# Kernel optimization log

Hardware: AMD Instinct MI355X
Metric: run time of the kernel (lower is better)

The kernel has to match this reference:

```python
import jax, jax.numpy as jnp
import numpy as np

B, IN, H = 16384, 1024, 1024


def setup_inputs() -> dict:
    key = jax.random.key(0)
    ks = jax.random.split(key, 16)
    stdv = 1.0 / np.sqrt(H)
    u = lambda k, shape: jax.random.uniform(k, shape, jnp.float32, -stdv, stdv)
    return {
        "input": jax.random.normal(ks[0], (B, IN), jnp.float32),
        "prev_h": jax.random.normal(ks[1], (B, H), jnp.float32),
        "prev_c": jax.random.normal(ks[2], (B, H), jnp.float32),
        "weight_xi": u(ks[3], (IN, H)), "weight_hi": u(ks[4], (H, H)),
        "weight_xf": u(ks[5], (IN, H)), "weight_hf": u(ks[6], (H, H)),
        "weight_xu": u(ks[7], (IN, H)), "weight_hu": u(ks[8], (H, H)),
        "weight_xo": u(ks[9], (IN, H)), "weight_ho": u(ks[10], (H, H)),
        "bias_i": u(ks[11], (H,)), "bias_f": u(ks[12], (H,)),
        "bias_o": u(ks[13], (H,)), "bias_u": u(ks[14], (H,)),
    }


def reference(input, prev_h, prev_c,
              weight_xi, weight_hi, weight_xf, weight_hf,
              weight_xu, weight_hu, weight_xo, weight_ho,
              bias_i, bias_f, bias_o, bias_u):
    i = jax.nn.sigmoid(input @ weight_xi + prev_h @ weight_hi + bias_i)
    f = jax.nn.sigmoid(input @ weight_xf + prev_h @ weight_hf + bias_f)
    o = jax.nn.sigmoid(input @ weight_xo + prev_h @ weight_ho + bias_o)
    u = jnp.tanh(input @ weight_xu + prev_h @ weight_hu + bias_u)
    c = f * prev_c + i * u
    h = o * jnp.tanh(c)
    return (h, c)
```

## Files before the change

kernel.cpp:

```cpp
#include <hip/hip_runtime.h>
#include <hip/hip_bf16.h>
#include <stdint.h>
#include <type_traits>


typedef short bf16x8 __attribute__((ext_vector_type(8)));
typedef unsigned short u16x8 __attribute__((ext_vector_type(8)));
typedef float f32x4 __attribute__((ext_vector_type(4)));

__device__ __forceinline__ unsigned short f2bf(float f) {
    union { float f; uint32_t u; } v; v.f = f;
    uint32_t r = v.u + 0x7FFFu + ((v.u >> 16) & 1u);
    return (unsigned short)(r >> 16);
}

__device__ __forceinline__ float fsig(float x) { return 1.0f / (1.0f + __expf(-x)); }
__device__ __forceinline__ float ftanh(float x) { return 2.0f * fsig(2.0f * x) - 1.0f; }

__global__ __launch_bounds__(256) void pack_a_kernel(const float* __restrict__ input,
                                                     const float* __restrict__ prev_h,
                                                     unsigned short* __restrict__ Apk) {
    long idx = (long)blockIdx.x * 256 + threadIdx.x;
    long e0 = idx * 8;
    int b = (int)(e0 >> 11);
    int k = (int)(e0 & 2047);
    const float* src = (k < 1024) ? (input + (size_t)b * 1024 + k)
                                  : (prev_h + (size_t)b * 1024 + (k - 1024));
    float4 lo = *(const float4*)src;
    float4 hi = *(const float4*)(src + 4);
    u16x8 o;
    o[0] = f2bf(lo.x); o[1] = f2bf(lo.y); o[2] = f2bf(lo.z); o[3] = f2bf(lo.w);
    o[4] = f2bf(hi.x); o[5] = f2bf(hi.y); o[6] = f2bf(hi.z); o[7] = f2bf(hi.w);
    *(u16x8*)(Apk + e0) = o;
}

__global__ __launch_bounds__(256) void pack_b_kernel(
        const float* __restrict__ wxi, const float* __restrict__ wxf,
        const float* __restrict__ wxo, const float* __restrict__ wxu,
        const float* __restrict__ whi, const float* __restrict__ whf,
        const float* __restrict__ who, const float* __restrict__ whu,
        unsigned short* __restrict__ Bpk) {
    int idx = blockIdx.x * 256 + threadIdx.x;
    int g  = idx >> 18;
    int r  = idx & 262143;
    int kc = r >> 10;
    int j  = r & 1023;
    const float* wx = (g == 0) ? wxi : (g == 1) ? wxf : (g == 2) ? wxo : wxu;
    const float* wh = (g == 0) ? whi : (g == 1) ? whf : (g == 2) ? who : whu;
    int k0 = kc * 8;
    const float* src = (k0 < 1024) ? (wx + (size_t)k0 * 1024 + j)
                                   : (wh + (size_t)(k0 - 1024) * 1024 + j);
    u16x8 o;
#pragma unroll
    for (int t = 0; t < 8; ++t) o[t] = f2bf(src[(size_t)t * 1024]);
    *(u16x8*)(Bpk + (((size_t)(g * 1024 + j)) << 11) + k0) = o;
}


#define GLL(gp, lp) __builtin_amdgcn_global_load_lds( \
        (__attribute__((address_space(1))) void*)(gp), \
        (__attribute__((address_space(3))) void*)(lp), 16, 0, 0)

#define BAR() do { asm volatile("" ::: "memory"); __builtin_amdgcn_s_barrier(); \
                   asm volatile("" ::: "memory"); } while (0)

__global__ __launch_bounds__(512, 2) void lstm_gemm_kernel(
        const unsigned short* __restrict__ Apk,
        const unsigned short* __restrict__ Bpk,
        const float* __restrict__ prev_c,
        const float* __restrict__ bi, const float* __restrict__ bf_,
        const float* __restrict__ bo, const float* __restrict__ bu,
        float* __restrict__ out_h, float* __restrict__ out_c) {
    __shared__ __align__(16) unsigned char smem[131072];
    const int tid = threadIdx.x;
    const int w = tid >> 6, l = tid & 63;
    const int lr = l & 15, s4 = l >> 4;
    const int wm = w >> 2, wq = w & 3;

    const int bid = blockIdx.x;
    const int sw = ((bid & 7) << 7) + (bid >> 3);
    const int tileRow = sw & 63, tileCol = sw >> 6;
    const int rowBase = tileRow * 256;
    const int jBase = tileCol * 64;

    const int swr = ((s4 ^ ((lr >> 1) & 3)) << 4);

    int aoff[8], boff[4];
#pragma unroll
    for (int m = 0; m < 8; ++m) aoff[m] = (wm * 128 + m * 16 + lr) * 64 + swr;
#pragma unroll
    for (int g = 0; g < 4; ++g) boff[g] = 16384 + (g * 64 + wq * 16 + lr) * 64 + swr;

    const int slot = (l & 3) ^ ((l >> 3) & 3);
    const int rloc = w * 16 + (l >> 2);
    const unsigned short* aSrc0 = Apk + (size_t)(rowBase + rloc) * 2048 + slot * 8;
    const unsigned short* aSrc1 = Apk + (size_t)(rowBase + 128 + rloc) * 2048 + slot * 8;
    const int br0 = rloc, br1 = 128 + rloc;
    const unsigned short* bSrc0 = Bpk + (((size_t)((br0 >> 6) * 1024 + jBase + (br0 & 63))) << 11) + slot * 8;
    const unsigned short* bSrc1 = Bpk + (((size_t)((br1 >> 6) * 1024 + jBase + (br1 & 63))) << 11) + slot * 8;
    const int aDst0 = w * 1024;
    const int aDst1 = 8192 + w * 1024;
    const int bDst0 = 16384 + w * 1024;
    const int bDst1 = 24576 + w * 1024;

#define STAGE_A2(T) do { const int _bb = ((T) & 3) * 32768; \
        GLL(aSrc0 + (size_t)(T) * 32, smem + _bb + aDst0); \
        GLL(aSrc1 + (size_t)(T) * 32, smem + _bb + aDst1); } while (0)
#define STAGE_B2(T) do { const int _bb = ((T) & 3) * 32768; \
        GLL(bSrc0 + (size_t)(T) * 32, smem + _bb + bDst0); \
        GLL(bSrc1 + (size_t)(T) * 32, smem + _bb + bDst1); } while (0)

    f32x4 acc[8][4];
    const f32x4 vzero = {0.f, 0.f, 0.f, 0.f};
#pragma unroll
    for (int m = 0; m < 8; ++m)
#pragma unroll
        for (int g = 0; g < 4; ++g) acc[m][g] = vzero;

    bf16x8 bvA[4], bvB[4];

    STAGE_A2(0); STAGE_B2(0);
    STAGE_A2(1); STAGE_B2(1);
    asm volatile("s_waitcnt vmcnt(4)" ::: "memory");
    BAR();

    auto slice = [&](int t, auto vnc, auto stgc, bf16x8 (&bv)[4]) {
        constexpr int VN = decltype(vnc)::value;
        constexpr bool STG = decltype(stgc)::value;
        const int bt = (t & 3) * 32768;
        bf16x8 av0[4];
#pragma unroll
        for (int m = 0; m < 4; ++m) av0[m] = *(const bf16x8*)(smem + bt + aoff[m]);
#pragma unroll
        for (int g = 0; g < 4; ++g) bv[g] = *(const bf16x8*)(smem + bt + boff[g]);
        if constexpr (STG) STAGE_A2(t + 2);
        BAR();
        asm volatile("s_waitcnt lgkmcnt(0)" ::: "memory");
        __builtin_amdgcn_sched_barrier(0);
        __builtin_amdgcn_s_setprio(1);
#pragma unroll
        for (int m = 0; m < 4; ++m)
#pragma unroll
            for (int g = 0; g < 4; ++g)
                acc[m][g] = __builtin_amdgcn_mfma_f32_16x16x32_bf16(av0[m], bv[g], acc[m][g], 0, 0, 0);
        __builtin_amdgcn_s_setprio(0);
        bf16x8 av1[4];
#pragma unroll
        for (int m = 0; m < 4; ++m) av1[m] = *(const bf16x8*)(smem + bt + aoff[4 + m]);
        if constexpr (STG) STAGE_B2(t + 2);
        if constexpr (VN == 4)      asm volatile("s_waitcnt vmcnt(4)" ::: "memory");
        else if constexpr (VN == 0) asm volatile("s_waitcnt vmcnt(0)" ::: "memory");
        BAR();
        asm volatile("s_waitcnt lgkmcnt(0)" ::: "memory");
        __builtin_amdgcn_sched_barrier(0);
        __builtin_amdgcn_s_setprio(1);
#pragma unroll
        for (int m = 0; m < 4; ++m)
#pragma unroll
            for (int g = 0; g < 4; ++g)
                acc[4 + m][g] = __builtin_amdgcn_mfma_f32_16x16x32_bf16(av1[m], bv[g], acc[4 + m][g], 0, 0, 0);
        __builtin_amdgcn_s_setprio(0);
    };

    using ci4 = std::integral_constant<int, 4>;
    using ci0 = std::integral_constant<int, 0>;
    using cim = std::integral_constant<int, -1>;
    using bt_ = std::integral_constant<bool, true>;
    using bf_c = std::integral_constant<bool, false>;

#pragma unroll 1
    for (int t = 0; t < 60; t += 2) {
        slice(t,     ci4{}, bt_{}, bvA);
        slice(t + 1, ci4{}, bt_{}, bvB);
    }
    slice(60, ci4{}, bt_{},  bvA);
    slice(61, ci4{}, bt_{},  bvB);
    slice(62, ci0{}, bf_c{}, bvA);
    slice(63, cim{}, bf_c{}, bvB);

    const int colIdx = jBase + wq * 16 + lr;
    const float vbi = bi[colIdx], vbf = bf_[colIdx], vbo = bo[colIdx], vbu = bu[colIdx];
    const int rowB = rowBase + wm * 128 + s4 * 4;
#pragma unroll
    for (int m = 0; m < 8; ++m) {
#pragma unroll
        for (int tt = 0; tt < 4; ++tt) {
            const size_t idx = (size_t)(rowB + m * 16 + tt) * 1024 + colIdx;
            float zi = acc[m][0][tt] + vbi;
            float zf = acc[m][1][tt] + vbf;
            float zo = acc[m][2][tt] + vbo;
            float zu = acc[m][3][tt] + vbu;
            float iv = fsig(zi), fv = fsig(zf), ov = fsig(zo), uv = ftanh(zu);
            float cv = fv * prev_c[idx] + iv * uv;
            out_c[idx] = cv;
            out_h[idx] = ov * ftanh(cv);
        }
    }
#undef STAGE_A2
#undef STAGE_B2
}

extern "C" void kernel_launch(void* const* d_in, const int* in_sizes, int n_in,
                              void* d_out, int out_size, void* d_ws, size_t ws_size,
                              hipStream_t stream) {
    const float* input  = (const float*)d_in[0];
    const float* prev_h = (const float*)d_in[1];
    const float* prev_c = (const float*)d_in[2];
    const float* wxi = (const float*)d_in[3];
    const float* whi = (const float*)d_in[4];
    const float* wxf = (const float*)d_in[5];
    const float* whf = (const float*)d_in[6];
    const float* wxu = (const float*)d_in[7];
    const float* whu = (const float*)d_in[8];
    const float* wxo = (const float*)d_in[9];
    const float* who = (const float*)d_in[10];
    const float* bi  = (const float*)d_in[11];
    const float* bf_ = (const float*)d_in[12];
    const float* bo  = (const float*)d_in[13];
    const float* bu  = (const float*)d_in[14];

    unsigned short* Apk = (unsigned short*)d_ws;
    unsigned short* Bpk = (unsigned short*)((char*)d_ws + (size_t)67108864);

    float* out_h = (float*)d_out;
    float* out_c = out_h + (size_t)16384 * 1024;

    pack_a_kernel<<<dim3(16384), dim3(256), 0, stream>>>(input, prev_h, Apk);
    pack_b_kernel<<<dim3(4096), dim3(256), 0, stream>>>(wxi, wxf, wxo, wxu,
                                                        whi, whf, who, whu, Bpk);
    lstm_gemm_kernel<<<dim3(1024), dim3(512), 0, stream>>>(Apk, Bpk, prev_c,
                                                           bi, bf_, bo, bu, out_h, out_c);
}
```

Measured before the change: 350.5 us.

## Simplify GEMM main loop to one barrier per K-slice with merged staging

Replaces the two-phase slice schedule with a single-phase one. The old schedule split the A loads across halves, used two barriers per slice, and used setprio and sched_barrier to interleave LDS reads, global-to-LDS staging and MFMA. Now each slice issues all four staging loads for slice t+2 up front, reads all A and B fragments, runs all 32 MFMAs, waits on vmcnt and hits one barrier. The aim is to halve barrier count and scheduling overhead, at the cost of the explicit LDS-read/MFMA overlap and the wave priority hints. More fragments live at once also raises register pressure.

```diff
diff --git a/kernel.cpp b/kernel.cpp
--- a/kernel.cpp
+++ b/kernel.cpp
@@ -103,10 +103,9 @@
     const int bDst0 = 16384 + w * 1024;
     const int bDst1 = 24576 + w * 1024;
 
-#define STAGE_A2(T) do { const int _bb = ((T) & 3) * 32768; \
+#define STAGE4(T) do { const int _bb = ((T) & 3) * 32768; \
         GLL(aSrc0 + (size_t)(T) * 32, smem + _bb + aDst0); \
-        GLL(aSrc1 + (size_t)(T) * 32, smem + _bb + aDst1); } while (0)
-#define STAGE_B2(T) do { const int _bb = ((T) & 3) * 32768; \
+        GLL(aSrc1 + (size_t)(T) * 32, smem + _bb + aDst1); \
         GLL(bSrc0 + (size_t)(T) * 32, smem + _bb + bDst0); \
         GLL(bSrc1 + (size_t)(T) * 32, smem + _bb + bDst1); } while (0)
 
@@ -117,66 +116,40 @@
 #pragma unroll
         for (int g = 0; g < 4; ++g) acc[m][g] = vzero;
 
-    bf16x8 bvA[4], bvB[4];
-
-    STAGE_A2(0); STAGE_B2(0);
-    STAGE_A2(1); STAGE_B2(1);
+    STAGE4(0); STAGE4(1);
     asm volatile("s_waitcnt vmcnt(4)" ::: "memory");
     BAR();
 
-    auto slice = [&](int t, auto vnc, auto stgc, bf16x8 (&bv)[4]) {
+    auto slice = [&](int t, auto vnc, auto stgc) {
         constexpr int VN = decltype(vnc)::value;
         constexpr bool STG = decltype(stgc)::value;
         const int bt = (t & 3) * 32768;
-        bf16x8 av0[4];
-#pragma unroll
-        for (int m = 0; m < 4; ++m) av0[m] = *(const bf16x8*)(smem + bt + aoff[m]);
+        if constexpr (STG) STAGE4(t + 2);
+        bf16x8 bv[4], av[8];
 #pragma unroll
         for (int g = 0; g < 4; ++g) bv[g] = *(const bf16x8*)(smem + bt + boff[g]);
-        if constexpr (STG) STAGE_A2(t + 2);
-        BAR();
-        asm volatile("s_waitcnt lgkmcnt(0)" ::: "memory");
-        __builtin_amdgcn_sched_barrier(0);
-        __builtin_amdgcn_s_setprio(1);
-#pragma unroll
-        for (int m = 0; m < 4; ++m)
+#pragma unroll
+        for (int m = 0; m < 8; ++m) av[m] = *(const bf16x8*)(smem + bt + aoff[m]);
+#pragma unroll
+        for (int m = 0; m < 8; ++m)
 #pragma unroll
             for (int g = 0; g < 4; ++g)
-                acc[m][g] = __builtin_amdgcn_mfma_f32_16x16x32_bf16(av0[m], bv[g], acc[m][g], 0, 0, 0);
-        __builtin_amdgcn_s_setprio(0);
-        bf16x8 av1[4];
-#pragma unroll
-        for (int m = 0; m < 4; ++m) av1[m] = *(const bf16x8*)(smem + bt + aoff[4 + m]);
-        if constexpr (STG) STAGE_B2(t + 2);
+                acc[m][g] = __builtin_amdgcn_mfma_f32_16x16x32_bf16(av[m], bv[g], acc[m][g], 0, 0, 0);
         if constexpr (VN == 4)      asm volatile("s_waitcnt vmcnt(4)" ::: "memory");
         else if constexpr (VN == 0) asm volatile("s_waitcnt vmcnt(0)" ::: "memory");
-        BAR();
-        asm volatile("s_waitcnt lgkmcnt(0)" ::: "memory");
-        __builtin_amdgcn_sched_barrier(0);
-        __builtin_amdgcn_s_setprio(1);
-#pragma unroll
-        for (int m = 0; m < 4; ++m)
-#pragma unroll
-            for (int g = 0; g < 4; ++g)
-                acc[4 + m][g] = __builtin_amdgcn_mfma_f32_16x16x32_bf16(av1[m], bv[g], acc[4 + m][g], 0, 0, 0);
-        __builtin_amdgcn_s_setprio(0);
+        if constexpr (VN >= 0) BAR();
     };
 
-    using ci4 = std::integral_constant<int, 4>;
-    using ci0 = std::integral_constant<int, 0>;
-    using cim = std::integral_constant<int, -1>;
-    using bt_ = std::integral_constant<bool, true>;
-    using bf_c = std::integral_constant<bool, false>;
+    using c4 = std::integral_constant<int, 4>;
+    using c0 = std::integral_constant<int, 0>;
+    using cm = std::integral_constant<int, -1>;
+    using bT = std::integral_constant<bool, true>;
+    using bF = std::integral_constant<bool, false>;
 
 #pragma unroll 1
-    for (int t = 0; t < 60; t += 2) {
-        slice(t,     ci4{}, bt_{}, bvA);
-        slice(t + 1, ci4{}, bt_{}, bvB);
-    }
-    slice(60, ci4{}, bt_{},  bvA);
-    slice(61, ci4{}, bt_{},  bvB);
-    slice(62, ci0{}, bf_c{}, bvA);
-    slice(63, cim{}, bf_c{}, bvB);
+    for (int t = 0; t < 62; ++t) slice(t, c4{}, bT{});
+    slice(62, c0{}, bF{});
+    slice(63, cm{}, bF{});
 
     const int colIdx = jBase + wq * 16 + lr;
     const float vbi = bi[colIdx], vbf = bf_[colIdx], vbo = bo[colIdx], vbu = bu[colIdx];
@@ -196,8 +169,7 @@
             out_h[idx] = ov * ftanh(cv);
         }
     }
-#undef STAGE_A2
-#undef STAGE_B2
+#undef STAGE4
 }
 
 extern "C" void kernel_launch(void* const* d_in, const int* in_sizes, int n_in,
```

Result: no change. 345.1 us (-1.5%).
